# Performance work log

Hardware: AMD Instinct MI355X
Metric: run time of the kernel (lower is better)

The kernel has to match this reference:

```python
import jax, jax.numpy as jnp
import numpy as np

K = 24            # kNN neighbors per DynamicEdgeConv (includes self, dist 0)
N_PER_GRAPH = 128 # uniform nodes per graph
N_GRAPHS = 128
N_IN = 16
HID = 128
N_OUT = 6


def _knn_idx(xg, k):
    # xg: [G, N, D] -> indices of k nearest neighbors per node, [G, N, k]
    sq = jnp.sum(xg * xg, axis=-1)                       # [G, N]
    d2 = sq[:, :, None] + sq[:, None, :] - 2.0 * jnp.einsum('gnd,gmd->gnm', xg, xg)
    _, idx = jax.lax.top_k(-d2, k)                       # smallest distances
    return idx


def _dynamic_edge_conv(xg, w, b, k=K):
    # DynamicEdgeConv: recompute kNN on current features, edge MLP on
    # [x_i, x_j - x_i], max-aggregate over neighbors.
    idx = _knn_idx(xg, k)                                # [G, N, k]
    x_j = jax.vmap(lambda v, i: v[i])(xg, idx)           # [G, N, k, D]
    x_i = xg[:, :, None, :]                              # [G, N, 1, D]
    e = jnp.concatenate([jnp.broadcast_to(x_i, x_j.shape), x_j - x_i], axis=-1)
    h = jax.nn.elu(jnp.einsum('gnkf,fh->gnkh', e, w) + b)
    return jnp.max(h, axis=2)                            # [G, N, H]


def _linear(x, w, b):
    return x @ w + b


def setup_inputs() -> dict:
    key = jax.random.key(0)
    ks = jax.random.split(key, 16)

    def W(k, fi, fo):
        return (jax.random.normal(k, (fi, fo), dtype=jnp.float32) / np.sqrt(fi)).astype(jnp.float32)

    inp = {
        'x_pf': jax.random.normal(ks[0], (N_GRAPHS * N_PER_GRAPH, N_IN), dtype=jnp.float32),
        'enc_w1': W(ks[1], N_IN, HID),  'enc_b1': jnp.zeros((HID,), jnp.float32),
        'enc_w2': W(ks[2], HID, HID),   'enc_b2': jnp.zeros((HID,), jnp.float32),
        'conv1_w': W(ks[3], 2 * HID, HID), 'conv1_b': jnp.zeros((HID,), jnp.float32),
        'conv2_w': W(ks[4], 2 * HID, HID), 'conv2_b': jnp.zeros((HID,), jnp.float32),
        'conv3_w': W(ks[5], 2 * HID, HID), 'conv3_b': jnp.zeros((HID,), jnp.float32),
        'out_w1': W(ks[6], HID, 64), 'out_b1': jnp.zeros((64,), jnp.float32),
        'out_w2': W(ks[7], 64, 32),  'out_b2': jnp.zeros((32,), jnp.float32),
        'out_w3': W(ks[8], 32, 32),  'out_b3': jnp.zeros((32,), jnp.float32),
        'out_w4': W(ks[9], 32, N_OUT), 'out_b4': jnp.zeros((N_OUT,), jnp.float32),
        'batch_pf': jnp.repeat(jnp.arange(N_GRAPHS, dtype=jnp.int64 if jax.config.jax_enable_x64 else jnp.int32), N_PER_GRAPH),
    }
    return inp


def reference(x_pf, enc_w1, enc_b1, enc_w2, enc_b2,
              conv1_w, conv1_b, conv2_w, conv2_b, conv3_w, conv3_b,
              out_w1, out_b1, out_w2, out_b2, out_w3, out_b3, out_w4, out_b4,
              batch_pf):
    G = x_pf.shape[0] // N_PER_GRAPH
    # pf_encode: Linear -> ELU -> Linear -> ELU
    h = jax.nn.elu(_linear(x_pf, enc_w1, enc_b1))
    h = jax.nn.elu(_linear(h, enc_w2, enc_b2))
    hg = h.reshape(G, N_PER_GRAPH, HID)  # uniform graphs; batch_pf = repeat(arange(G))
    hg = _dynamic_edge_conv(hg, conv1_w, conv1_b)
    hg = _dynamic_edge_conv(hg, conv2_w, conv2_b)
    hg = _dynamic_edge_conv(hg, conv3_w, conv3_b)
    # global_add_pool over nodes of each graph
    pooled = jnp.sum(hg, axis=1)                          # [G, HID]
    o = jax.nn.elu(_linear(pooled, out_w1, out_b1))
    o = jax.nn.elu(_linear(o, out_w2, out_b2))
    o = jax.nn.elu(_linear(o, out_w3, out_b3))
    o = _linear(o, out_w4, out_b4)
    return (o, batch_pf)
```

## Files before the change

kernel.cpp:

```cpp
#include <hip/hip_runtime.h>
#include <hip/hip_fp16.h>
#include <hip/hip_bf16.h>
#include <cmath>

#define G_NUM 128
#define NPTS  128
#define FDIM  128
#define KNNK  24
#define NTOT  (G_NUM*NPTS)

typedef short s8v __attribute__((ext_vector_type(8)));
typedef float f32x4 __attribute__((ext_vector_type(4)));

__device__ __forceinline__ float eluf(float x){ return x > 0.0f ? x : expm1f(x); }

__device__ __forceinline__ unsigned short f2bf(float f) {
    unsigned int u = __float_as_uint(f);
    unsigned int r = (u + 0x7fffu + ((u >> 16) & 1u)) >> 16;
    return (unsigned short)r;
}
__device__ __forceinline__ float bf2f(unsigned short b) {
    return __uint_as_float(((unsigned int)b) << 16);
}

__global__ void prep_kernel(const float* __restrict__ w1, const float* __restrict__ w2,
                            const float* __restrict__ w3, const float* __restrict__ ew2,
                            const float* __restrict__ b1, const float* __restrict__ b2,
                            const float* __restrict__ b3,
                            unsigned short* __restrict__ wcatT,
                            unsigned short* __restrict__ enc2T,
                            float* __restrict__ bias,
                            const int* __restrict__ bpf,
                            float* __restrict__ out)
{
    int e = blockIdx.x * 256 + threadIdx.x;
    if (e < 16384) out[768 + e] = (float)bpf[e];
    if (e < 98304) {
        int l = e >> 15;
        int r = e & 32767;
        int k = r >> 8;
        int n = r & 255;
        const float* w = (l == 0) ? w1 : ((l == 1) ? w2 : w3);
        float v = (n < 128) ? (w[k * 128 + n] - w[(128 + k) * 128 + n])
                            : w[(128 + k) * 128 + (n - 128)];
        wcatT[l * 32768 + n * 128 + k] = f2bf(v);
    } else if (e < 114688) {
        int i = e - 98304;
        int k = i >> 7, n = i & 127;
        enc2T[n * 128 + k] = f2bf(ew2[k * 128 + n]);
    } else if (e < 115456) {
        int j = e - 114688;
        int l = j >> 8, c = j & 255;
        const float* b = (l == 0) ? b1 : ((l == 1) ? b2 : b3);
        bias[l * 256 + c] = (c < 128) ? b[c] : 0.0f;
    }
}

template<int DOELU>
__global__ __launch_bounds__(256) void gemmT(const float* __restrict__ A,
                                             const unsigned short* __restrict__ Bt,
                                             const float* __restrict__ bias,
                                             float* __restrict__ C0)
{
    extern __shared__ char smc[];
    const int tid = threadIdx.x;
    const int m0 = blockIdx.x * 128;
    float* C = C0;

    for (int e = tid; e < 4096; e += 256) {
        int m = e >> 5, q = e & 31;
        float4 v = *reinterpret_cast<const float4*>(&A[(size_t)(m0 + m) * 128 + 4 * q]);
        ushort4 p;
        p.x = f2bf(v.x); p.y = f2bf(v.y); p.z = f2bf(v.z); p.w = f2bf(v.w);
        int byte = (m * 256 + q * 8) ^ ((m & 15) << 4);
        *reinterpret_cast<ushort4*>(smc + byte) = p;
    }
    for (int e = tid; e < 2048; e += 256) {
        int n = e >> 4, q = e & 15;
        uint4 v = *reinterpret_cast<const uint4*>(Bt + n * 128 + q * 8);
        int byte = (n * 256 + q * 16) ^ ((n & 15) << 4);
        *reinterpret_cast<uint4*>(smc + 32768 + byte) = v;
    }
    __syncthreads();

    const int l = tid & 63, w = tid >> 6;
    const int wr = w >> 1, wc = w & 1;
    const int lr = l & 15, lg = l >> 4;

    f32x4 acc[4][4] = {};
    #pragma unroll
    for (int ks = 0; ks < 4; ++ks) {
        s8v a_f[4], b_f[4];
        #pragma unroll
        for (int mi = 0; mi < 4; ++mi) {
            int row = wr * 64 + mi * 16 + lr;
            int byte = (row * 256 + ks * 64 + lg * 16) ^ ((row & 15) << 4);
            a_f[mi] = *reinterpret_cast<const s8v*>(smc + byte);
        }
        #pragma unroll
        for (int ni = 0; ni < 4; ++ni) {
            int n = wc * 64 + ni * 16 + lr;
            int byte = (n * 256 + ks * 64 + lg * 16) ^ ((n & 15) << 4);
            b_f[ni] = *reinterpret_cast<const s8v*>(smc + 32768 + byte);
        }
        #pragma unroll
        for (int mi = 0; mi < 4; ++mi)
            #pragma unroll
            for (int ni = 0; ni < 4; ++ni)
                acc[mi][ni] = __builtin_amdgcn_mfma_f32_16x16x32_bf16(
                    a_f[mi], b_f[ni], acc[mi][ni], 0, 0, 0);
    }

    float bl[4];
    #pragma unroll
    for (int ni = 0; ni < 4; ++ni) bl[ni] = bias[wc * 64 + ni * 16 + lr];

    #pragma unroll
    for (int mi = 0; mi < 4; ++mi) {
        int rbase = m0 + wr * 64 + mi * 16 + lg * 4;
        #pragma unroll
        for (int ni = 0; ni < 4; ++ni) {
            int col = wc * 64 + ni * 16 + lr;
            #pragma unroll
            for (int q = 0; q < 4; ++q) {
                float v = acc[mi][ni][q] + bl[ni];
                if (DOELU) v = eluf(v);
                C[(size_t)(rbase + q) * 128 + col] = v;
            }
        }
    }
}

template<int KD, int TM, int DOELU>
__global__ __launch_bounds__(256) void gemm2(const float* __restrict__ A, int lda,
                                             const float* __restrict__ B, int ldb,
                                             const float* __restrict__ bias,
                                             float* __restrict__ C0)
{
    extern __shared__ float sm[];
    float* As = sm;
    float* Bs = sm + TM * (KD + 1);
    const int tid = threadIdx.x;
    const int m0 = blockIdx.x * TM;
    float* C = C0;
    const float* bg = bias;

    constexpr int NF4 = KD / 4;
    for (int e = tid; e < TM * NF4; e += 256) {
        int q = e % NF4, m = e / NF4;
        float4 v = *reinterpret_cast<const float4*>(&A[(size_t)(m0 + m) * lda + 4 * q]);
        float* dst = &As[m * (KD + 1) + 4 * q];
        dst[0] = v.x; dst[1] = v.y; dst[2] = v.z; dst[3] = v.w;
    }
    for (int e = tid; e < KD * 32; e += 256) {
        int q = e & 31, k = e >> 5;
        float4 v = *reinterpret_cast<const float4*>(&B[(size_t)k * ldb + 4 * q]);
        float* dst = &Bs[k * 129 + 4 * q];
        dst[0] = v.x; dst[1] = v.y; dst[2] = v.z; dst[3] = v.w;
    }
    __syncthreads();

    const int tml = tid & 15;
    const int tnh = tid >> 4;
    constexpr int NR = TM / 16;
    float acc[NR][8] = {};
    #pragma unroll 4
    for (int k = 0; k < KD; ++k) {
        float av[NR], bv[8];
        #pragma unroll
        for (int s = 0; s < NR; ++s) av[s] = As[(tml + 16 * s) * (KD + 1) + k];
        #pragma unroll
        for (int u = 0; u < 8; ++u) bv[u] = Bs[k * 129 + tnh + 16 * u];
        #pragma unroll
        for (int s = 0; s < NR; ++s)
            #pragma unroll
            for (int u = 0; u < 8; ++u) acc[s][u] += av[s] * bv[u];
    }
    __syncthreads();
    float* Ce = sm;
    #pragma unroll
    for (int s = 0; s < NR; ++s)
        #pragma unroll
        for (int u = 0; u < 8; ++u)
            Ce[(tml + 16 * s) * 132 + tnh + 16 * u] = acc[s][u];
    __syncthreads();
    for (int e = tid; e < TM * 32; e += 256) {
        int q = e & 31, m = e >> 5;
        float4 v = *reinterpret_cast<const float4*>(&Ce[m * 132 + 4 * q]);
        float4 b4 = *reinterpret_cast<const float4*>(&bg[4 * q]);
        v.x += b4.x; v.y += b4.y; v.z += b4.z; v.w += b4.w;
        if (DOELU) { v.x = eluf(v.x); v.y = eluf(v.y); v.z = eluf(v.z); v.w = eluf(v.w); }
        *reinterpret_cast<float4*>(&C[(size_t)(m0 + m) * 128 + 4 * q]) = v;
    }
}

#define XHI_OFF 0
#define XLO_OFF 32768
#define D_OFF   65536
#define CC_OFF  98816
#define IDX_OFF 132608
#define SQ_OFF  138752
#define CONV_LDS 139264

__global__ __launch_bounds__(512) void conv_fused(const float* __restrict__ hin,
                                                  const unsigned short* __restrict__ wT,
                                                  const float* __restrict__ bias,
                                                  float* __restrict__ hout)
{
    extern __shared__ char smc[];
    float* D  = (float*)(smc + D_OFF);
    float* Sq = (float*)(smc + SQ_OFF);
    unsigned int* idxL = (unsigned int*)(smc + IDX_OFF);
    unsigned int* Cc   = (unsigned int*)(smc + CC_OFF);
    float* Al = (float*)(smc + XLO_OFF);

    const int g = blockIdx.x >> 1, half = blockIdx.x & 1;
    const int r0 = half * 64;
    const int tid = threadIdx.x;
    const float* hg = hin + (size_t)g * NPTS * FDIM;
    float* og = hout + (size_t)g * NPTS * FDIM;

    {
        const int m = tid >> 2;
        const int k0 = (tid & 3) * 32;
        float sq = 0.f;
        #pragma unroll
        for (int i = 0; i < 8; ++i) {
            float4 v = *reinterpret_cast<const float4*>(&hg[m * 128 + k0 + 4 * i]);
            ushort4 hi, lo;
            hi.x = f2bf(v.x); lo.x = f2bf(v.x - bf2f(hi.x));
            hi.y = f2bf(v.y); lo.y = f2bf(v.y - bf2f(hi.y));
            hi.z = f2bf(v.z); lo.z = f2bf(v.z - bf2f(hi.z));
            hi.w = f2bf(v.w); lo.w = f2bf(v.w - bf2f(hi.w));
            sq += v.x * v.x + v.y * v.y + v.z * v.z + v.w * v.w;
            int byte = (m * 256 + (k0 + 4 * i) * 2) ^ ((m & 15) << 4);
            *reinterpret_cast<ushort4*>(smc + XHI_OFF + byte) = hi;
            *reinterpret_cast<ushort4*>(smc + XLO_OFF + byte) = lo;
        }
        sq += __shfl_xor(sq, 1);
        sq += __shfl_xor(sq, 2);
        if ((tid & 3) == 0) Sq[m] = sq;
    }
    __syncthreads();

    const int l = tid & 63, w = tid >> 6;
    const int lr = l & 15, lg = l >> 4;

    if (w < 4) {
        const int arow = r0 + w * 16 + lr;
        const int aswz = (arow & 15) << 4;
        f32x4 acc[8] = {};
        #pragma unroll
        for (int ks = 0; ks < 4; ++ks) {
            int abyte = (arow * 256 + ks * 64 + lg * 16) ^ aswz;
            s8v ahi = *reinterpret_cast<const s8v*>(smc + XHI_OFF + abyte);
            s8v alo = *reinterpret_cast<const s8v*>(smc + XLO_OFF + abyte);
            #pragma unroll
            for (int ni = 0; ni < 8; ++ni) {
                int brow = ni * 16 + lr;
                int bbyte = (brow * 256 + ks * 64 + lg * 16) ^ ((brow & 15) << 4);
                s8v bhi = *reinterpret_cast<const s8v*>(smc + XHI_OFF + bbyte);
                s8v blo = *reinterpret_cast<const s8v*>(smc + XLO_OFF + bbyte);
                acc[ni] = __builtin_amdgcn_mfma_f32_16x16x32_bf16(alo, bhi, acc[ni], 0, 0, 0);
                acc[ni] = __builtin_amdgcn_mfma_f32_16x16x32_bf16(ahi, blo, acc[ni], 0, 0, 0);
                acc[ni] = __builtin_amdgcn_mfma_f32_16x16x32_bf16(ahi, bhi, acc[ni], 0, 0, 0);
            }
        }
        float sqa[4];
        #pragma unroll
        for (int q = 0; q < 4; ++q) sqa[q] = Sq[r0 + w * 16 + lg * 4 + q];
        #pragma unroll
        for (int ni = 0; ni < 8; ++ni) {
            float sqc = Sq[ni * 16 + lr];
            #pragma unroll
            for (int q = 0; q < 4; ++q)
                D[(w * 16 + lg * 4 + q) * 130 + ni * 16 + lr] =
                    sqa[q] + sqc - 2.f * acc[ni][q];
        }
    } else {
        const int w4 = w - 4;
        f32x4 acc[2][8] = {};
        #pragma unroll
        for (int ks = 0; ks < 4; ++ks) {
            s8v a_f[2];
            #pragma unroll
            for (int m2 = 0; m2 < 2; ++m2) {
                int row = (2 * w4 + m2) * 16 + lr;
                int byte = (row * 256 + ks * 64 + lg * 16) ^ ((row & 15) << 4);
                a_f[m2] = *reinterpret_cast<const s8v*>(smc + XHI_OFF + byte);
            }
            #pragma unroll
            for (int ni = 0; ni < 8; ++ni) {
                int n = 128 + ni * 16 + lr;
                s8v b = *reinterpret_cast<const s8v*>(wT + n * 128 + ks * 32 + lg * 8);
                #pragma unroll
                for (int m2 = 0; m2 < 2; ++m2)
                    acc[m2][ni] = __builtin_amdgcn_mfma_f32_16x16x32_bf16(
                        a_f[m2], b, acc[m2][ni], 0, 0, 0);
            }
        }
        #pragma unroll
        for (int m2 = 0; m2 < 2; ++m2)
            #pragma unroll
            for (int ni = 0; ni < 8; ++ni)
                #pragma unroll
                for (int q = 0; q < 4; ++q) {
                    float v = acc[m2][ni][q];
                    float p = __shfl_xor(v, 1);
                    if (!(lr & 1)) {
                        unsigned int u =
                            ((unsigned int)__half_as_ushort(__float2half(p)) << 16)
                          |  (unsigned int)__half_as_ushort(__float2half(v));
                        int j = (2 * w4 + m2) * 16 + lg * 4 + q;
                        Cc[j * 66 + ni * 8 + (lr >> 1)] = u;
                    }
                }
    }
    __syncthreads();

    {
        const int mt = w >> 1;
        const int nb = (w & 1) * 4;
        f32x4 acc[4] = {};
        const int arow = r0 + mt * 16 + lr;
        const int aswz = (arow & 15) << 4;
        #pragma unroll
        for (int ks = 0; ks < 4; ++ks) {
            int abyte = (arow * 256 + ks * 64 + lg * 16) ^ aswz;
            s8v a_f = *reinterpret_cast<const s8v*>(smc + XHI_OFF + abyte);
            #pragma unroll
            for (int ni = 0; ni < 4; ++ni) {
                int n = (nb + ni) * 16 + lr;
                s8v b = *reinterpret_cast<const s8v*>(wT + n * 128 + ks * 32 + lg * 8);
                acc[ni] = __builtin_amdgcn_mfma_f32_16x16x32_bf16(a_f, b, acc[ni], 0, 0, 0);
            }
        }
        #pragma unroll
        for (int ni = 0; ni < 4; ++ni) {
            int h = (nb + ni) * 16 + lr;
            float bl = bias[h];
            #pragma unroll
            for (int q = 0; q < 4; ++q)
                Al[(mt * 16 + lg * 4 + q) * 128 + h] = acc[ni][q] + bl;
        }
    }

    for (int lr2 = w * 8; lr2 < w * 8 + 8; ++lr2) {
        float2 cur = *reinterpret_cast<const float2*>(&D[lr2 * 130 + 2 * l]);
        unsigned int ub0 = __float_as_uint(cur.x);
        unsigned int ub1 = __float_as_uint(cur.y);
        unsigned int u0 = (ub0 & 0x80000000u) ? ~ub0 : (ub0 | 0x80000000u);
        unsigned int u1 = (ub1 & 0x80000000u) ? ~ub1 : (ub1 | 0x80000000u);

        bool c0 = true, c1 = true, in0 = false, in1 = false;
        int need = KNNK;
        for (int b = 31; b >= 0; --b) {
            bool z0 = c0 && !((u0 >> b) & 1u);
            bool z1 = c1 && !((u1 >> b) & 1u);
            int cnt = __popcll(__ballot(z0)) + __popcll(__ballot(z1));
            if (cnt > need) { c0 = z0; c1 = z1; }
            else if (cnt == need) { in0 |= z0; in1 |= z1; need = 0; break; }
            else { in0 |= z0; in1 |= z1; need -= cnt;
                   c0 = c0 && !z0; c1 = c1 && !z1; }
        }
        if (need > 0) {
            unsigned long long m0 = __ballot(c0), m1 = __ballot(c1);
            unsigned long long below = (1ull << l) - 1ull;
            int rk0 = __popcll(m0 & below) + __popcll(m1 & below);
            int rk1 = rk0 + (int)((m0 >> l) & 1ull);
            in0 = in0 || (c0 && rk0 < need);
            in1 = in1 || (c1 && rk1 < need);
        }
        unsigned long long f0 = __ballot(in0), f1 = __ballot(in1);
        int cnt0 = __popcll(f0);
        unsigned long long below = (1ull << l) - 1ull;
        if (in0) idxL[lr2 * KNNK + __popcll(f0 & below)] = 2 * l;
        if (in1) idxL[lr2 * KNNK + cnt0 + __popcll(f1 & below)] = 2 * l + 1;
    }
    __syncthreads();

    {
        const int hh = l >> 5, jl = l & 31;
        #pragma unroll
        for (int u = 0; u < 4; ++u) {
            const int r = w * 8 + 2 * u + hh;
            const unsigned int* il = &idxL[r * KNNK];
            float mc0 = -3.0e38f, mc1 = -3.0e38f, mc2 = -3.0e38f, mc3 = -3.0e38f;
            #pragma unroll
            for (int t = 0; t < KNNK; t += 4) {
                unsigned int p0 = il[t], p1 = il[t + 1], p2 = il[t + 2], p3 = il[t + 3];
                uint2 a = *reinterpret_cast<const uint2*>(&Cc[p0 * 66 + 2 * jl]);
                uint2 b = *reinterpret_cast<const uint2*>(&Cc[p1 * 66 + 2 * jl]);
                uint2 c = *reinterpret_cast<const uint2*>(&Cc[p2 * 66 + 2 * jl]);
                uint2 d = *reinterpret_cast<const uint2*>(&Cc[p3 * 66 + 2 * jl]);
                mc0 = fmaxf(fmaxf(mc0,
                        __half2float(__ushort_as_half((unsigned short)(a.x & 0xffffu)))),
                        fmaxf(__half2float(__ushort_as_half((unsigned short)(b.x & 0xffffu))),
                              fmaxf(__half2float(__ushort_as_half((unsigned short)(c.x & 0xffffu))),
                                    __half2float(__ushort_as_half((unsigned short)(d.x & 0xffffu))))));
                mc1 = fmaxf(fmaxf(mc1,
                        __half2float(__ushort_as_half((unsigned short)(a.x >> 16)))),
                        fmaxf(__half2float(__ushort_as_half((unsigned short)(b.x >> 16))),
                              fmaxf(__half2float(__ushort_as_half((unsigned short)(c.x >> 16))),
                                    __half2float(__ushort_as_half((unsigned short)(d.x >> 16))))));
                mc2 = fmaxf(fmaxf(mc2,
                        __half2float(__ushort_as_half((unsigned short)(a.y & 0xffffu)))),
                        fmaxf(__half2float(__ushort_as_half((unsigned short)(b.y & 0xffffu))),
                              fmaxf(__half2float(__ushort_as_half((unsigned short)(c.y & 0xffffu))),
                                    __half2float(__ushort_as_half((unsigned short)(d.y & 0xffffu))))));
                mc3 = fmaxf(fmaxf(mc3,
                        __half2float(__ushort_as_half((unsigned short)(a.y >> 16)))),
                        fmaxf(__half2float(__ushort_as_half((unsigned short)(b.y >> 16))),
                              fmaxf(__half2float(__ushort_as_half((unsigned short)(c.y >> 16))),
                                    __half2float(__ushort_as_half((unsigned short)(d.y >> 16))))));
            }
            float4 av = *reinterpret_cast<const float4*>(&Al[r * 128 + 4 * jl]);
            float4 o;
            o.x = eluf(av.x + mc0);
            o.y = eluf(av.y + mc1);
            o.z = eluf(av.z + mc2);
            o.w = eluf(av.w + mc3);
            *reinterpret_cast<float4*>(&og[(r0 + r) * 128 + 4 * jl]) = o;
        }
    }
}

__global__ __launch_bounds__(512) void head_kernel(const float* __restrict__ h,
        const float* __restrict__ w1, const float* __restrict__ b1,
        const float* __restrict__ w2, const float* __restrict__ b2,
        const float* __restrict__ w3, const float* __restrict__ b3,
        const float* __restrict__ w4, const float* __restrict__ b4,
        float* __restrict__ out)
{
    __shared__ float ps[4][128];
    __shared__ float pooled[128], s1[64], s2[32], s3[32];
    const int g = blockIdx.x, t = threadIdx.x;
    const float* hg = h + (size_t)g * NPTS * FDIM;
    const int f = t & 127, hp = t >> 7;
    float s = 0.0f;
    for (int p = 0; p < 32; ++p) s += hg[(hp * 32 + p) * 128 + f];
    ps[hp][f] = s;
    __syncthreads();
    if (t < 128) pooled[t] = ps[0][t] + ps[1][t] + ps[2][t] + ps[3][t];
    __syncthreads();
    if (t < 64) {
        float a = b1[t];
        #pragma unroll 8
        for (int k = 0; k < 128; ++k) a += pooled[k] * w1[k * 64 + t];
        s1[t] = eluf(a);
    }
    __syncthreads();
    if (t < 32) {
        float a = b2[t];
        #pragma unroll 8
        for (int k = 0; k < 64; ++k) a += s1[k] * w2[k * 32 + t];
        s2[t] = eluf(a);
    }
    __syncthreads();
    if (t < 32) {
        float a = b3[t];
        #pragma unroll 8
        for (int k = 0; k < 32; ++k) a += s2[k] * w3[k * 32 + t];
        s3[t] = eluf(a);
    }
    __syncthreads();
    if (t < 6) {
        float a = b4[t];
        #pragma unroll 8
        for (int k = 0; k < 32; ++k) a += s3[k] * w4[k * 6 + t];
        out[g * 6 + t] = a;
    }
}

extern "C" void kernel_launch(void* const* d_in, const int* in_sizes, int n_in,
                              void* d_out, int out_size, void* d_ws, size_t ws_size,
                              hipStream_t stream)
{
    const float* x_pf   = (const float*)d_in[0];
    const float* enc_w1 = (const float*)d_in[1];
    const float* enc_b1 = (const float*)d_in[2];
    const float* enc_w2 = (const float*)d_in[3];
    const float* enc_b2 = (const float*)d_in[4];
    const float* c1w = (const float*)d_in[5];
    const float* c1b = (const float*)d_in[6];
    const float* c2w = (const float*)d_in[7];
    const float* c2b = (const float*)d_in[8];
    const float* c3w = (const float*)d_in[9];
    const float* c3b = (const float*)d_in[10];
    const float* o_w1 = (const float*)d_in[11];
    const float* o_b1 = (const float*)d_in[12];
    const float* o_w2 = (const float*)d_in[13];
    const float* o_b2 = (const float*)d_in[14];
    const float* o_w3 = (const float*)d_in[15];
    const float* o_b3 = (const float*)d_in[16];
    const float* o_w4 = (const float*)d_in[17];
    const float* o_b4 = (const float*)d_in[18];
    const int*   bpf  = (const int*)d_in[19];
    float* out = (float*)d_out;

    float* ws   = (float*)d_ws;
    float* h_a  = ws;
    float* h_b  = h_a + (size_t)NTOT * FDIM;
    float* ac_c = h_b + (size_t)NTOT * FDIM;
    unsigned short* wcatT = (unsigned short*)(ac_c + (size_t)NTOT * FDIM);
    unsigned short* enc2T = wcatT + 3 * 32768;
    float* biasF = (float*)(enc2T + 16384);

    prep_kernel<<<451, 256, 0, stream>>>(c1w, c2w, c3w, enc_w2,
                                         c1b, c2b, c3b, wcatT, enc2T, biasF,
                                         bpf, out);

    gemm2<16, 64, 1><<<dim3(NTOT / 64, 1), 256, 8448 * 4, stream>>>(
        x_pf, 16, enc_w1, 128, enc_b1, ac_c);
    gemmT<1><<<dim3(NTOT / 128, 1), 256, 65536, stream>>>(
        ac_c, enc2T, enc_b2, h_a);

    float* hc = h_a;
    float* hn = h_b;
    for (int l = 0; l < 3; ++l) {
        conv_fused<<<2 * G_NUM, 512, CONV_LDS, stream>>>(
            hc, wcatT + (size_t)l * 32768, biasF + l * 256, hn);
        float* t = hc; hc = hn; hn = t;
    }

    head_kernel<<<G_NUM, 512, 0, stream>>>(hc, o_w1, o_b1, o_w2, o_b2, o_w3, o_b3,
                                           o_w4, o_b4, out);
}
```

Before: 292.5 us.

## Fuse encoder GEMMs, double conv block threads, fold pooling into last conv

The two encoder GEMMs are merged into one kernel that keeps the first layer's activations in LDS as bf16 and feeds them straight into MFMA, so the intermediate global buffer goes away. conv_fused now runs with 1024 threads per block, giving each wave a smaller share of the kNN distance, edge-projection and aggregation work. It also remaps the block-to-graph assignment and swizzles the LDS buffer that holds the per-node linear term. The last conv layer no longer writes node features; it sums them into per-half-graph partial pools, so the head kernel only adds two partials. The cost is higher register pressure per thread under launch_bounds(1024,4), plus an extra barrier inside the pooling branch.

```diff
diff --git a/kernel.cpp b/kernel.cpp
--- a/kernel.cpp
+++ b/kernel.cpp
@@ -56,141 +56,70 @@
     }
 }
 
-template<int DOELU>
-__global__ __launch_bounds__(256) void gemmT(const float* __restrict__ A,
-                                             const unsigned short* __restrict__ Bt,
-                                             const float* __restrict__ bias,
-                                             float* __restrict__ C0)
+#define E_XS  0
+#define E_W1  4352
+#define E_A   12544
+__global__ __launch_bounds__(512) void enc_fused(const float* __restrict__ x_pf,
+                                                 const float* __restrict__ w1,
+                                                 const float* __restrict__ b1,
+                                                 const unsigned short* __restrict__ e2T,
+                                                 const float* __restrict__ b2,
+                                                 float* __restrict__ hout)
 {
-    extern __shared__ char smc[];
+    __shared__ char smc[28928];
+    float* xs  = (float*)(smc + E_XS);
+    float* ws1 = (float*)(smc + E_W1);
     const int tid = threadIdx.x;
-    const int m0 = blockIdx.x * 128;
-    float* C = C0;
-
-    for (int e = tid; e < 4096; e += 256) {
-        int m = e >> 5, q = e & 31;
-        float4 v = *reinterpret_cast<const float4*>(&A[(size_t)(m0 + m) * 128 + 4 * q]);
-        ushort4 p;
-        p.x = f2bf(v.x); p.y = f2bf(v.y); p.z = f2bf(v.z); p.w = f2bf(v.w);
-        int byte = (m * 256 + q * 8) ^ ((m & 15) << 4);
-        *reinterpret_cast<ushort4*>(smc + byte) = p;
-    }
-    for (int e = tid; e < 2048; e += 256) {
-        int n = e >> 4, q = e & 15;
-        uint4 v = *reinterpret_cast<const uint4*>(Bt + n * 128 + q * 8);
-        int byte = (n * 256 + q * 16) ^ ((n & 15) << 4);
-        *reinterpret_cast<uint4*>(smc + 32768 + byte) = v;
-    }
-    __syncthreads();
-
-    const int l = tid & 63, w = tid >> 6;
-    const int wr = w >> 1, wc = w & 1;
-    const int lr = l & 15, lg = l >> 4;
-
-    f32x4 acc[4][4] = {};
-    #pragma unroll
-    for (int ks = 0; ks < 4; ++ks) {
-        s8v a_f[4], b_f[4];
-        #pragma unroll
-        for (int mi = 0; mi < 4; ++mi) {
-            int row = wr * 64 + mi * 16 + lr;
-            int byte = (row * 256 + ks * 64 + lg * 16) ^ ((row & 15) << 4);
-            a_f[mi] = *reinterpret_cast<const s8v*>(smc + byte);
+    const int m0 = blockIdx.x * 64;
+
+    for (int e = tid; e < 1024; e += 512) {
+        int m = e >> 4, k = e & 15;
+        xs[m * 17 + k] = x_pf[(size_t)(m0 + m) * 16 + k];
+    }
+    for (int e = tid; e < 2048; e += 512) ws1[e] = w1[e];
+    __syncthreads();
+
+    {
+        const int h = tid & 127, mg = tid >> 7;
+        float bb = b1[h];
+        #pragma unroll
+        for (int i = 0; i < 16; ++i) {
+            int m = mg * 16 + i;
+            float a = bb;
+            #pragma unroll
+            for (int k = 0; k < 16; ++k) a += xs[m * 17 + k] * ws1[k * 128 + h];
+            a = eluf(a);
+            int byte = (m * 256 + h * 2) ^ ((m & 15) << 4);
+            *reinterpret_cast<unsigned short*>(smc + E_A + byte) = f2bf(a);
+        }
+    }
+    __syncthreads();
+
+    {
+        const int l = tid & 63, w = tid >> 6;
+        const int lr = l & 15, lg = l >> 4;
+        const int mt = w >> 1, nh = w & 1;
+        f32x4 acc[4] = {};
+        #pragma unroll
+        for (int ks = 0; ks < 4; ++ks) {
+            int row = mt * 16 + lr;
+            int abyte = (row * 256 + ks * 64 + lg * 16) ^ ((row & 15) << 4);
+            s8v a_f = *reinterpret_cast<const s8v*>(smc + E_A + abyte);
+            #pragma unroll
+            for (int ni = 0; ni < 4; ++ni) {
+                int n = nh * 64 + ni * 16 + lr;
+                s8v b = *reinterpret_cast<const s8v*>(e2T + n * 128 + ks * 32 + lg * 8);
+                acc[ni] = __builtin_amdgcn_mfma_f32_16x16x32_bf16(a_f, b, acc[ni], 0, 0, 0);
+            }
         }
         #pragma unroll
         for (int ni = 0; ni < 4; ++ni) {
-            int n = wc * 64 + ni * 16 + lr;
-            int byte = (n * 256 + ks * 64 + lg * 16) ^ ((n & 15) << 4);
-            b_f[ni] = *reinterpret_cast<const s8v*>(smc + 32768 + byte);
-        }
-        #pragma unroll
-        for (int mi = 0; mi < 4; ++mi)
-            #pragma unroll
-            for (int ni = 0; ni < 4; ++ni)
-                acc[mi][ni] = __builtin_amdgcn_mfma_f32_16x16x32_bf16(
-                    a_f[mi], b_f[ni], acc[mi][ni], 0, 0, 0);
-    }
-
-    float bl[4];
-    #pragma unroll
-    for (int ni = 0; ni < 4; ++ni) bl[ni] = bias[wc * 64 + ni * 16 + lr];
-
-    #pragma unroll
-    for (int mi = 0; mi < 4; ++mi) {
-        int rbase = m0 + wr * 64 + mi * 16 + lg * 4;
-        #pragma unroll
-        for (int ni = 0; ni < 4; ++ni) {
-            int col = wc * 64 + ni * 16 + lr;
-            #pragma unroll
-            for (int q = 0; q < 4; ++q) {
-                float v = acc[mi][ni][q] + bl[ni];
-                if (DOELU) v = eluf(v);
-                C[(size_t)(rbase + q) * 128 + col] = v;
-            }
-        }
-    }
-}
-
-template<int KD, int TM, int DOELU>
-__global__ __launch_bounds__(256) void gemm2(const float* __restrict__ A, int lda,
-                                             const float* __restrict__ B, int ldb,
-                                             const float* __restrict__ bias,
-                                             float* __restrict__ C0)
-{
-    extern __shared__ float sm[];
-    float* As = sm;
-    float* Bs = sm + TM * (KD + 1);
-    const int tid = threadIdx.x;
-    const int m0 = blockIdx.x * TM;
-    float* C = C0;
-    const float* bg = bias;
-
-    constexpr int NF4 = KD / 4;
-    for (int e = tid; e < TM * NF4; e += 256) {
-        int q = e % NF4, m = e / NF4;
-        float4 v = *reinterpret_cast<const float4*>(&A[(size_t)(m0 + m) * lda + 4 * q]);
-        float* dst = &As[m * (KD + 1) + 4 * q];
-        dst[0] = v.x; dst[1] = v.y; dst[2] = v.z; dst[3] = v.w;
-    }
-    for (int e = tid; e < KD * 32; e += 256) {
-        int q = e & 31, k = e >> 5;
-        float4 v = *reinterpret_cast<const float4*>(&B[(size_t)k * ldb + 4 * q]);
-        float* dst = &Bs[k * 129 + 4 * q];
-        dst[0] = v.x; dst[1] = v.y; dst[2] = v.z; dst[3] = v.w;
-    }
-    __syncthreads();
-
-    const int tml = tid & 15;
-    const int tnh = tid >> 4;
-    constexpr int NR = TM / 16;
-    float acc[NR][8] = {};
-    #pragma unroll 4
-    for (int k = 0; k < KD; ++k) {
-        float av[NR], bv[8];
-        #pragma unroll
-        for (int s = 0; s < NR; ++s) av[s] = As[(tml + 16 * s) * (KD + 1) + k];
-        #pragma unroll
-        for (int u = 0; u < 8; ++u) bv[u] = Bs[k * 129 + tnh + 16 * u];
-        #pragma unroll
-        for (int s = 0; s < NR; ++s)
-            #pragma unroll
-            for (int u = 0; u < 8; ++u) acc[s][u] += av[s] * bv[u];
-    }
-    __syncthreads();
-    float* Ce = sm;
-    #pragma unroll
-    for (int s = 0; s < NR; ++s)
-        #pragma unroll
-        for (int u = 0; u < 8; ++u)
-            Ce[(tml + 16 * s) * 132 + tnh + 16 * u] = acc[s][u];
-    __syncthreads();
-    for (int e = tid; e < TM * 32; e += 256) {
-        int q = e & 31, m = e >> 5;
-        float4 v = *reinterpret_cast<const float4*>(&Ce[m * 132 + 4 * q]);
-        float4 b4 = *reinterpret_cast<const float4*>(&bg[4 * q]);
-        v.x += b4.x; v.y += b4.y; v.z += b4.z; v.w += b4.w;
-        if (DOELU) { v.x = eluf(v.x); v.y = eluf(v.y); v.z = eluf(v.z); v.w = eluf(v.w); }
-        *reinterpret_cast<float4*>(&C[(size_t)(m0 + m) * 128 + 4 * q]) = v;
+            int n = nh * 64 + ni * 16 + lr;
+            float bl = b2[n];
+            #pragma unroll
+            for (int q = 0; q < 4; ++q)
+                hout[(size_t)(m0 + mt * 16 + lg * 4 + q) * 128 + n] = eluf(acc[ni][q] + bl);
+        }
     }
 }
 
@@ -202,30 +131,34 @@
 #define SQ_OFF  138752
 #define CONV_LDS 139264
 
-__global__ __launch_bounds__(512) void conv_fused(const float* __restrict__ hin,
-                                                  const unsigned short* __restrict__ wT,
-                                                  const float* __restrict__ bias,
-                                                  float* __restrict__ hout)
+template<int POOL>
+__global__ __launch_bounds__(1024, 4) void conv_fused(const float* __restrict__ hin,
+                                                      const unsigned short* __restrict__ wT,
+                                                      const float* __restrict__ bias,
+                                                      float* __restrict__ hout,
+                                                      float* __restrict__ ppool)
 {
     extern __shared__ char smc[];
     float* D  = (float*)(smc + D_OFF);
+    float* pp = (float*)(smc + D_OFF);
     float* Sq = (float*)(smc + SQ_OFF);
     unsigned int* idxL = (unsigned int*)(smc + IDX_OFF);
     unsigned int* Cc   = (unsigned int*)(smc + CC_OFF);
-    float* Al = (float*)(smc + XLO_OFF);
-
-    const int g = blockIdx.x >> 1, half = blockIdx.x & 1;
-    const int r0 = half * 64;
+
+    const int bid = blockIdx.x;
+    const int g  = (bid & 7) * 16 + (bid >> 4);
+    const int hf = (bid >> 3) & 1;
+    const int r0 = hf * 64;
     const int tid = threadIdx.x;
     const float* hg = hin + (size_t)g * NPTS * FDIM;
     float* og = hout + (size_t)g * NPTS * FDIM;
 
     {
-        const int m = tid >> 2;
-        const int k0 = (tid & 3) * 32;
+        const int m = tid >> 3;
+        const int k0 = (tid & 7) * 16;
         float sq = 0.f;
         #pragma unroll
-        for (int i = 0; i < 8; ++i) {
+        for (int i = 0; i < 4; ++i) {
             float4 v = *reinterpret_cast<const float4*>(&hg[m * 128 + k0 + 4 * i]);
             ushort4 hi, lo;
             hi.x = f2bf(v.x); lo.x = f2bf(v.x - bf2f(hi.x));
@@ -239,25 +172,28 @@
         }
         sq += __shfl_xor(sq, 1);
         sq += __shfl_xor(sq, 2);
-        if ((tid & 3) == 0) Sq[m] = sq;
+        sq += __shfl_xor(sq, 4);
+        if ((tid & 7) == 0) Sq[m] = sq;
     }
     __syncthreads();
 
     const int l = tid & 63, w = tid >> 6;
     const int lr = l & 15, lg = l >> 4;
 
-    if (w < 4) {
-        const int arow = r0 + w * 16 + lr;
+    if (w < 8) {
+        const int t2 = w >> 1;
+        const int nh = w & 1;
+        const int arow = r0 + t2 * 16 + lr;
         const int aswz = (arow & 15) << 4;
-        f32x4 acc[8] = {};
+        f32x4 acc[4] = {};
         #pragma unroll
         for (int ks = 0; ks < 4; ++ks) {
             int abyte = (arow * 256 + ks * 64 + lg * 16) ^ aswz;
             s8v ahi = *reinterpret_cast<const s8v*>(smc + XHI_OFF + abyte);
             s8v alo = *reinterpret_cast<const s8v*>(smc + XLO_OFF + abyte);
             #pragma unroll
-            for (int ni = 0; ni < 8; ++ni) {
-                int brow = ni * 16 + lr;
+            for (int ni = 0; ni < 4; ++ni) {
+                int brow = (nh * 4 + ni) * 16 + lr;
                 int bbyte = (brow * 256 + ks * 64 + lg * 16) ^ ((brow & 15) << 4);
                 s8v bhi = *reinterpret_cast<const s8v*>(smc + XHI_OFF + bbyte);
                 s8v blo = *reinterpret_cast<const s8v*>(smc + XLO_OFF + bbyte);
@@ -268,84 +204,78 @@
         }
         float sqa[4];
         #pragma unroll
-        for (int q = 0; q < 4; ++q) sqa[q] = Sq[r0 + w * 16 + lg * 4 + q];
-        #pragma unroll
-        for (int ni = 0; ni < 8; ++ni) {
-            float sqc = Sq[ni * 16 + lr];
+        for (int q = 0; q < 4; ++q) sqa[q] = Sq[r0 + t2 * 16 + lg * 4 + q];
+        #pragma unroll
+        for (int ni = 0; ni < 4; ++ni) {
+            int col = (nh * 4 + ni) * 16 + lr;
+            float sqc = Sq[col];
             #pragma unroll
             for (int q = 0; q < 4; ++q)
-                D[(w * 16 + lg * 4 + q) * 130 + ni * 16 + lr] =
-                    sqa[q] + sqc - 2.f * acc[ni][q];
+                D[(t2 * 16 + lg * 4 + q) * 130 + col] = sqa[q] + sqc - 2.f * acc[ni][q];
         }
     } else {
-        const int w4 = w - 4;
-        f32x4 acc[2][8] = {};
+        const int jt = w - 8;
+        f32x4 acc[8] = {};
         #pragma unroll
         for (int ks = 0; ks < 4; ++ks) {
-            s8v a_f[2];
-            #pragma unroll
-            for (int m2 = 0; m2 < 2; ++m2) {
-                int row = (2 * w4 + m2) * 16 + lr;
-                int byte = (row * 256 + ks * 64 + lg * 16) ^ ((row & 15) << 4);
-                a_f[m2] = *reinterpret_cast<const s8v*>(smc + XHI_OFF + byte);
-            }
+            int row = jt * 16 + lr;
+            int byte = (row * 256 + ks * 64 + lg * 16) ^ ((row & 15) << 4);
+            s8v a_f = *reinterpret_cast<const s8v*>(smc + XHI_OFF + byte);
             #pragma unroll
             for (int ni = 0; ni < 8; ++ni) {
                 int n = 128 + ni * 16 + lr;
                 s8v b = *reinterpret_cast<const s8v*>(wT + n * 128 + ks * 32 + lg * 8);
-                #pragma unroll
-                for (int m2 = 0; m2 < 2; ++m2)
-                    acc[m2][ni] = __builtin_amdgcn_mfma_f32_16x16x32_bf16(
-                        a_f[m2], b, acc[m2][ni], 0, 0, 0);
-            }
-        }
-        #pragma unroll
-        for (int m2 = 0; m2 < 2; ++m2)
-            #pragma unroll
-            for (int ni = 0; ni < 8; ++ni)
-                #pragma unroll
-                for (int q = 0; q < 4; ++q) {
-                    float v = acc[m2][ni][q];
-                    float p = __shfl_xor(v, 1);
-                    if (!(lr & 1)) {
-                        unsigned int u =
-                            ((unsigned int)__half_as_ushort(__float2half(p)) << 16)
-                          |  (unsigned int)__half_as_ushort(__float2half(v));
-                        int j = (2 * w4 + m2) * 16 + lg * 4 + q;
-                        Cc[j * 66 + ni * 8 + (lr >> 1)] = u;
-                    }
+                acc[ni] = __builtin_amdgcn_mfma_f32_16x16x32_bf16(a_f, b, acc[ni], 0, 0, 0);
+            }
+        }
+        #pragma unroll
+        for (int ni = 0; ni < 8; ++ni)
+            #pragma unroll
+            for (int q = 0; q < 4; ++q) {
+                float v = acc[ni][q];
+                float p = __shfl_xor(v, 1);
+                if (!(lr & 1)) {
+                    unsigned int u =
+                        ((unsigned int)__half_as_ushort(__float2half(p)) << 16)
+                      |  (unsigned int)__half_as_ushort(__float2half(v));
+                    int j = jt * 16 + lg * 4 + q;
+                    Cc[j * 66 + ni * 8 + (lr >> 1)] = u;
                 }
+            }
     }
     __syncthreads();
 
     {
-        const int mt = w >> 1;
-        const int nb = (w & 1) * 4;
-        f32x4 acc[4] = {};
+        const int mt = w >> 2;
+        const int nb = (w & 3) * 2;
         const int arow = r0 + mt * 16 + lr;
         const int aswz = (arow & 15) << 4;
+        f32x4 acc[2] = {};
         #pragma unroll
         for (int ks = 0; ks < 4; ++ks) {
             int abyte = (arow * 256 + ks * 64 + lg * 16) ^ aswz;
             s8v a_f = *reinterpret_cast<const s8v*>(smc + XHI_OFF + abyte);
             #pragma unroll
-            for (int ni = 0; ni < 4; ++ni) {
+            for (int ni = 0; ni < 2; ++ni) {
                 int n = (nb + ni) * 16 + lr;
                 s8v b = *reinterpret_cast<const s8v*>(wT + n * 128 + ks * 32 + lg * 8);
                 acc[ni] = __builtin_amdgcn_mfma_f32_16x16x32_bf16(a_f, b, acc[ni], 0, 0, 0);
             }
         }
         #pragma unroll
-        for (int ni = 0; ni < 4; ++ni) {
+        for (int ni = 0; ni < 2; ++ni) {
             int h = (nb + ni) * 16 + lr;
             float bl = bias[h];
             #pragma unroll
-            for (int q = 0; q < 4; ++q)
-                Al[(mt * 16 + lg * 4 + q) * 128 + h] = acc[ni][q] + bl;
-        }
-    }
-
-    for (int lr2 = w * 8; lr2 < w * 8 + 8; ++lr2) {
+            for (int q = 0; q < 4; ++q) {
+                int row = mt * 16 + lg * 4 + q;
+                int byte = (row * 512 + h * 4) ^ ((row & 3) << 4);
+                *reinterpret_cast<float*>(smc + XLO_OFF + byte) = acc[ni][q] + bl;
+            }
+        }
+    }
+
+    for (int lr2 = w * 4; lr2 < w * 4 + 4; ++lr2) {
         float2 cur = *reinterpret_cast<const float2*>(&D[lr2 * 130 + 2 * l]);
         unsigned int ub0 = __float_as_uint(cur.x);
         unsigned int ub1 = __float_as_uint(cur.y);
@@ -381,9 +311,10 @@
 
     {
         const int hh = l >> 5, jl = l & 31;
-        #pragma unroll
-        for (int u = 0; u < 4; ++u) {
-            const int r = w * 8 + 2 * u + hh;
+        float4 ps = {0.f, 0.f, 0.f, 0.f};
+        #pragma unroll
+        for (int u = 0; u < 2; ++u) {
+            const int r = w * 4 + 2 * u + hh;
             const unsigned int* il = &idxL[r * KNNK];
             float mc0 = -3.0e38f, mc1 = -3.0e38f, mc2 = -3.0e38f, mc3 = -3.0e38f;
             #pragma unroll
@@ -414,34 +345,42 @@
                               fmaxf(__half2float(__ushort_as_half((unsigned short)(c.y >> 16))),
                                     __half2float(__ushort_as_half((unsigned short)(d.y >> 16))))));
             }
-            float4 av = *reinterpret_cast<const float4*>(&Al[r * 128 + 4 * jl]);
+            int abyte = (r * 512 + 16 * jl) ^ ((r & 3) << 4);
+            float4 av = *reinterpret_cast<const float4*>(smc + XLO_OFF + abyte);
             float4 o;
             o.x = eluf(av.x + mc0);
             o.y = eluf(av.y + mc1);
             o.z = eluf(av.z + mc2);
             o.w = eluf(av.w + mc3);
-            *reinterpret_cast<float4*>(&og[(r0 + r) * 128 + 4 * jl]) = o;
-        }
-    }
-}
-
-__global__ __launch_bounds__(512) void head_kernel(const float* __restrict__ h,
+            if (!POOL) {
+                *reinterpret_cast<float4*>(&og[(r0 + r) * 128 + 4 * jl]) = o;
+            } else {
+                ps.x += o.x; ps.y += o.y; ps.z += o.z; ps.w += o.w;
+            }
+        }
+        if (POOL) {
+            *reinterpret_cast<float4*>(&pp[(w * 2 + hh) * 132 + 4 * jl]) = ps;
+            __syncthreads();
+            if (tid < 128) {
+                float s = 0.f;
+                #pragma unroll 8
+                for (int rg = 0; rg < 32; ++rg) s += pp[rg * 132 + tid];
+                ppool[(g * 2 + hf) * 128 + tid] = s;
+            }
+        }
+    }
+}
+
+__global__ __launch_bounds__(128) void head_kernel(const float* __restrict__ ppool,
         const float* __restrict__ w1, const float* __restrict__ b1,
         const float* __restrict__ w2, const float* __restrict__ b2,
         const float* __restrict__ w3, const float* __restrict__ b3,
         const float* __restrict__ w4, const float* __restrict__ b4,
         float* __restrict__ out)
 {
-    __shared__ float ps[4][128];
     __shared__ float pooled[128], s1[64], s2[32], s3[32];
     const int g = blockIdx.x, t = threadIdx.x;
-    const float* hg = h + (size_t)g * NPTS * FDIM;
-    const int f = t & 127, hp = t >> 7;
-    float s = 0.0f;
-    for (int p = 0; p < 32; ++p) s += hg[(hp * 32 + p) * 128 + f];
-    ps[hp][f] = s;
-    __syncthreads();
-    if (t < 128) pooled[t] = ps[0][t] + ps[1][t] + ps[2][t] + ps[3][t];
+    pooled[t] = ppool[(2 * g) * 128 + t] + ppool[(2 * g + 1) * 128 + t];
     __syncthreads();
     if (t < 64) {
         float a = b1[t];
@@ -501,8 +440,8 @@
     float* ws   = (float*)d_ws;
     float* h_a  = ws;
     float* h_b  = h_a + (size_t)NTOT * FDIM;
-    float* ac_c = h_b + (size_t)NTOT * FDIM;
-    unsigned short* wcatT = (unsigned short*)(ac_c + (size_t)NTOT * FDIM);
+    float* ppool = h_b + (size_t)NTOT * FDIM;
+    unsigned short* wcatT = (unsigned short*)(ppool + 256 * 128);
     unsigned short* enc2T = wcatT + 3 * 32768;
     float* biasF = (float*)(enc2T + 16384);
 
@@ -510,19 +449,16 @@
                                          c1b, c2b, c3b, wcatT, enc2T, biasF,
                                          bpf, out);
 
-    gemm2<16, 64, 1><<<dim3(NTOT / 64, 1), 256, 8448 * 4, stream>>>(
-        x_pf, 16, enc_w1, 128, enc_b1, ac_c);
-    gemmT<1><<<dim3(NTOT / 128, 1), 256, 65536, stream>>>(
-        ac_c, enc2T, enc_b2, h_a);
-
-    float* hc = h_a;
-    float* hn = h_b;
-    for (int l = 0; l < 3; ++l) {
-        conv_fused<<<2 * G_NUM, 512, CONV_LDS, stream>>>(
-            hc, wcatT + (size_t)l * 32768, biasF + l * 256, hn);
-        float* t = hc; hc = hn; hn = t;
-    }
-
-    head_kernel<<<G_NUM, 512, 0, stream>>>(hc, o_w1, o_b1, o_w2, o_b2, o_w3, o_b3,
-                                           o_w4, o_b4, out);
-}
+    enc_fused<<<NTOT / 64, 512, 0, stream>>>(x_pf, enc_w1, enc_b1,
+                                             enc2T, enc_b2, h_a);
+
+    conv_fused<0><<<2 * G_NUM, 1024, CONV_LDS, stream>>>(
+        h_a, wcatT, biasF, h_b, ppool);
+    conv_fused<0><<<2 * G_NUM, 1024, CONV_LDS, stream>>>(
+        h_b, wcatT + 32768, biasF + 256, h_a, ppool);
+    conv_fused<1><<<2 * G_NUM, 1024, CONV_LDS, stream>>>(
+        h_a, wcatT + 65536, biasF + 512, h_b, ppool);
+
+    head_kernel<<<G_NUM, 128, 0, stream>>>(ppool, o_w1, o_b1, o_w2, o_b2,
+                                           o_w3, o_b3, o_w4, o_b4, out);
+}
```

Measured after the change: 257.9 us. 1.13x faster.
